# Kernel optimization log

Measured on AMD Instinct MI355X. Metric: run time of the kernel, lower is better.

The kernel has to match this reference:

```python
import jax, jax.numpy as jnp
import numpy as np

K_LAYERS = 10
ALPHA = 0.1
N_NODES = 100000
N_EDGES = 500000
N_PATHS = 3
D = 128
HID = 128


def setup_inputs() -> dict:
    key = jax.random.key(0)
    k1, k2, k3, k4 = jax.random.split(key, 4)
    h = jax.random.normal(k1, (N_NODES, D), dtype=jnp.float32)
    edges = jax.random.randint(k2, (N_PATHS, 2, N_EDGES), 0, N_NODES, dtype=jnp.int64)
    W1 = jax.random.normal(k3, (D, HID), dtype=jnp.float32) * (1.0 / np.sqrt(D))
    b1 = jnp.zeros((HID,), dtype=jnp.float32)
    w2 = jax.random.normal(k4, (HID, 1), dtype=jnp.float32) * (1.0 / np.sqrt(HID))
    return {"h": h, "edges": edges, "W1": W1, "b1": b1, "w2": w2}


def _appnp(h0, src, dst):
    # DGL APPNPConv (eval mode, no dropout): symmetric degree normalization,
    # K steps of h <- (1-alpha) * D_in^{-1/2} A D_out^{-1/2} h + alpha * h0
    n = h0.shape[0]
    ones = jnp.ones(src.shape[0], dtype=h0.dtype)
    out_deg = jnp.clip(jax.ops.segment_sum(ones, src, num_segments=n), 1.0)
    in_deg = jnp.clip(jax.ops.segment_sum(ones, dst, num_segments=n), 1.0)
    norm_s = out_deg ** -0.5  # [N]
    norm_d = in_deg ** -0.5   # [N]

    def step(x, _):
        msg = (x * norm_s[:, None])[src]                       # [E, D] gather
        agg = jax.ops.segment_sum(msg, dst, num_segments=n)    # [N, D] scatter-add
        x = (1.0 - ALPHA) * (agg * norm_d[:, None]) + ALPHA * h0
        return x, None

    x, _ = jax.lax.scan(step, h0, None, length=K_LAYERS)
    return x


def reference(h, edges, W1, b1, w2):
    src = edges[:, 0, :]  # [P, E]
    dst = edges[:, 1, :]
    # one APPNP propagation per meta-path, vmapped over the P axis
    z = jax.vmap(lambda s, d: _appnp(h, s, d))(src, dst)  # [P, N, D]
    z = jnp.transpose(z, (1, 0, 2))                        # [N, P, D]
    # semantic attention: small MLP -> mean over nodes -> softmax over paths
    w = jnp.tanh(z @ W1 + b1) @ w2   # [N, P, 1]
    w = w.mean(axis=0)               # [P, 1]
    beta = jax.nn.softmax(w, axis=0) # [P, 1]
    return (beta[None, :, :] * z).sum(axis=1)  # [N, D]
```

## Files before the change

kernel.cpp:

```cpp
#include <hip/hip_runtime.h>
#include <math.h>

#define N_NODES 100000
#define N_EDGES 500000
#define N_PATHS 3
#define DIM 128
#define K_LAYERS 10
#define NBLK_PER_PATH ((N_NODES + 255) / 256)

typedef __attribute__((ext_vector_type(8))) short bf16x8;
typedef __attribute__((ext_vector_type(4))) float f32x4;

__global__ __launch_bounds__(256) void deg_kernel(const int* __restrict__ edges,
                                                  int* __restrict__ degS,
                                                  int* __restrict__ degD) {
    int idx = blockIdx.x * 256 + threadIdx.x;
    if (idx < N_PATHS * N_EDGES) {
        int p = idx / N_EDGES;
        int e = idx - p * N_EDGES;
        const int* src = edges + (size_t)p * 2 * N_EDGES;
        const int* dst = src + N_EDGES;
        atomicAdd(&degS[p * N_NODES + src[e]], 1);
        atomicAdd(&degD[p * N_NODES + dst[e]], 1);
    }
}

__global__ __launch_bounds__(256) void norm_kernel(const int* __restrict__ degS,
                                                   const int* __restrict__ degD,
                                                   float* __restrict__ norm_s,
                                                   float* __restrict__ norm_d) {
    int n = blockIdx.x * 256 + threadIdx.x;
    if (n < N_PATHS * N_NODES) {
        norm_s[n] = 1.0f / sqrtf(fmaxf((float)degS[n], 1.0f));
        norm_d[n] = 1.0f / sqrtf(fmaxf((float)degD[n], 1.0f));
    }
}

__global__ __launch_bounds__(256) void blocksum_kernel(const int* __restrict__ cnt,
                                                       int* __restrict__ bsum) {
    int b = blockIdx.x;
    int p = b / NBLK_PER_PATH;
    int lb = b - p * NBLK_PER_PATH;
    int idx = lb * 256 + threadIdx.x;
    int v = (idx < N_NODES) ? cnt[p * N_NODES + idx] : 0;
#pragma unroll
    for (int off = 32; off; off >>= 1) v += __shfl_xor(v, off);
    __shared__ int ws[4];
    if ((threadIdx.x & 63) == 0) ws[threadIdx.x >> 6] = v;
    __syncthreads();
    if (threadIdx.x == 0) bsum[b] = ws[0] + ws[1] + ws[2] + ws[3];
}

__global__ __launch_bounds__(512) void bscan_kernel(int* __restrict__ bsum) {
    __shared__ int s[512];
    int p = blockIdx.x;
    int t = threadIdx.x;
    int v = (t < NBLK_PER_PATH) ? bsum[p * NBLK_PER_PATH + t] : 0;
    s[t] = v;
    __syncthreads();
    for (int off = 1; off < 512; off <<= 1) {
        int x = s[t];
        int a = (t >= off) ? s[t - off] : 0;
        __syncthreads();
        s[t] = x + a;
        __syncthreads();
    }
    if (t < NBLK_PER_PATH) bsum[p * NBLK_PER_PATH + t] = s[t] - v;
}

__global__ __launch_bounds__(256) void scan_write_kernel(const int* __restrict__ cnt,
                                                         const int* __restrict__ bsum,
                                                         int* __restrict__ row_ptr_all,
                                                         int* __restrict__ cursor_all) {
    __shared__ int s[256];
    int b = blockIdx.x;
    int p = b / NBLK_PER_PATH;
    int lb = b - p * NBLK_PER_PATH;
    int idx = lb * 256 + threadIdx.x;
    int t = threadIdx.x;
    int v = (idx < N_NODES) ? cnt[p * N_NODES + idx] : 0;
    s[t] = v;
    __syncthreads();
    for (int off = 1; off < 256; off <<= 1) {
        int x = s[t];
        int a = (t >= off) ? s[t - off] : 0;
        __syncthreads();
        s[t] = x + a;
        __syncthreads();
    }
    int excl = s[t] - v + bsum[b];
    if (idx < N_NODES) {
        row_ptr_all[p * (N_NODES + 1) + idx] = excl;
        cursor_all[p * N_NODES + idx] = excl;
        if (idx == N_NODES - 1)
            row_ptr_all[p * (N_NODES + 1) + N_NODES] = excl + v;
    }
}

__global__ __launch_bounds__(256) void fill_kernel(const int* __restrict__ edges,
                                                   const float* __restrict__ norm_s,
                                                   const float* __restrict__ norm_d,
                                                   int* __restrict__ cursor,
                                                   int2* __restrict__ cw) {
    int idx = blockIdx.x * 256 + threadIdx.x;
    if (idx < N_PATHS * N_EDGES) {
        int p = idx / N_EDGES;
        int e = idx - p * N_EDGES;
        const int* src = edges + (size_t)p * 2 * N_EDGES;
        const int* dst = src + N_EDGES;
        int s = src[e], d = dst[e];
        int pos = atomicAdd(&cursor[p * N_NODES + d], 1);
        float w = 0.9f * norm_s[p * N_NODES + s] * norm_d[p * N_NODES + d];
        cw[(size_t)p * N_EDGES + pos] = make_int2(s, __float_as_int(w));
    }
}

__device__ __forceinline__ unsigned bf16pack(float a, float b) {
    unsigned ua = __float_as_uint(a), ub = __float_as_uint(b);
    ua = (ua + 0x7fffu + ((ua >> 16) & 1)) >> 16;
    ub = (ub + 0x7fffu + ((ub >> 16) & 1)) >> 16;
    return ua | (ub << 16);
}

__global__ __launch_bounds__(256) void cast_kernel(const float4* __restrict__ in,
                                                   ushort4* __restrict__ outp) {
    int idx = blockIdx.x * 256 + threadIdx.x;
    if (idx < N_NODES * DIM / 4) {
        float4 v = in[idx];
        ushort4 o;
        unsigned u;
        u = __float_as_uint(v.x); o.x = (unsigned short)((u + 0x7fff + ((u >> 16) & 1)) >> 16);
        u = __float_as_uint(v.y); o.y = (unsigned short)((u + 0x7fff + ((u >> 16) & 1)) >> 16);
        u = __float_as_uint(v.z); o.z = (unsigned short)((u + 0x7fff + ((u >> 16) & 1)) >> 16);
        u = __float_as_uint(v.w); o.w = (unsigned short)((u + 0x7fff + ((u >> 16) & 1)) >> 16);
        outp[idx] = o;
    }
}

__global__ __launch_bounds__(256) void w1t_kernel(const float* __restrict__ W1,
                                                  unsigned short* __restrict__ W1t) {
    int idx = blockIdx.x * 256 + threadIdx.x;
    if (idx < DIM * DIM) {
        int c = idx >> 7, k = idx & 127;
        unsigned u = __float_as_uint(W1[k * DIM + c]);
        W1t[idx] = (unsigned short)((u + 0x7fff + ((u >> 16) & 1)) >> 16);
    }
}

template <int OUT_F32>
__global__ __launch_bounds__(256) void prop_kernel(const unsigned short* __restrict__ xin,
                                                   size_t in_stride,
                                                   const float* __restrict__ h0f,
                                                   void* __restrict__ xout,
                                                   const int* __restrict__ row_ptr,
                                                   const int2* __restrict__ cw) {
    int wid  = threadIdx.x >> 6;
    int lane = threadIdx.x & 63;
    int q    = lane >> 4;
    int ql   = lane & 15;
    int nodeBase = blockIdx.x * 16 + wid * 4;
    int p  = nodeBase / N_NODES;
    int nb = nodeBase - p * N_NODES;
    const int*  rp   = row_ptr + p * (N_NODES + 1);
    const int2* cwp  = cw + (size_t)p * N_EDGES;
    const uint4* xin4 = (const uint4*)(xin + (size_t)p * in_stride);

    int rv = 0;
    if (lane < 5) rv = rp[nb + lane];
    int beg = __shfl(rv, q);
    int end = __shfl(rv, q + 1);
    int deg = end - beg;
    int myNode = nb + q;
    int maxd = deg;
    maxd = max(maxd, __shfl_xor(maxd, 16));
    maxd = max(maxd, __shfl_xor(maxd, 32));

    float a0 = 0.f, a1 = 0.f, a2 = 0.f, a3 = 0.f;
    float a4 = 0.f, a5 = 0.f, a6 = 0.f, a7 = 0.f;

    for (int base = 0; base < maxd; base += 16) {
        int2 e = make_int2(0, 0);
        if (base + ql < deg) e = cwp[beg + base + ql];
        int lim = maxd - base; if (lim > 16) lim = 16;
#pragma unroll 4
        for (int j = 0; j < lim; ++j) {
            int lsrc = (lane & 48) | j;
            int   c = __shfl(e.x, lsrc);
            float w = __int_as_float(__shfl(e.y, lsrc));
            if (base + j < deg) {
                uint4 v = xin4[(size_t)c * 16 + ql];
                a0 = fmaf(w, __uint_as_float(v.x << 16), a0);
                a1 = fmaf(w, __uint_as_float(v.x & 0xffff0000u), a1);
                a2 = fmaf(w, __uint_as_float(v.y << 16), a2);
                a3 = fmaf(w, __uint_as_float(v.y & 0xffff0000u), a3);
                a4 = fmaf(w, __uint_as_float(v.z << 16), a4);
                a5 = fmaf(w, __uint_as_float(v.z & 0xffff0000u), a5);
                a6 = fmaf(w, __uint_as_float(v.w << 16), a6);
                a7 = fmaf(w, __uint_as_float(v.w & 0xffff0000u), a7);
            }
        }
    }

    const float4* h4 = (const float4*)(h0f + (size_t)myNode * DIM);
    float4 h0v = h4[ql * 2];
    float4 h1v = h4[ql * 2 + 1];
    a0 += 0.1f * h0v.x; a1 += 0.1f * h0v.y; a2 += 0.1f * h0v.z; a3 += 0.1f * h0v.w;
    a4 += 0.1f * h1v.x; a5 += 0.1f * h1v.y; a6 += 0.1f * h1v.z; a7 += 0.1f * h1v.w;

    size_t row = (size_t)p * N_NODES + myNode;
    if (OUT_F32) {
        float4* zo = (float4*)xout + row * 32;
        zo[ql * 2]     = make_float4(a0, a1, a2, a3);
        zo[ql * 2 + 1] = make_float4(a4, a5, a6, a7);
    } else {
        uint4 o;
        o.x = bf16pack(a0, a1);
        o.y = bf16pack(a2, a3);
        o.z = bf16pack(a4, a5);
        o.w = bf16pack(a6, a7);
        ((uint4*)xout)[row * 16 + ql] = o;
    }
}

__device__ __forceinline__ float fast_tanh(float x) {
    float e = __expf(2.0f * x);
    return 1.0f - 2.0f / (e + 1.0f);
}

__global__ __launch_bounds__(256) void attn_kernel(const float* __restrict__ z,
                                                   const unsigned short* __restrict__ W1t,
                                                   const float* __restrict__ b1,
                                                   const float* __restrict__ w2,
                                                   float* __restrict__ wsum) {
    const int wid  = threadIdx.x >> 6;
    const int lane = threadIdx.x & 63;
    const int c0   = lane & 15;
    const int kh   = lane >> 4;

    const bf16x8* w1t8 = (const bf16x8*)W1t;
    bf16x8 Bf[8][4];
#pragma unroll
    for (int nt = 0; nt < 8; ++nt)
#pragma unroll
        for (int ks = 0; ks < 4; ++ks)
            Bf[nt][ks] = w1t8[(nt * 16 + c0) * 16 + ks * 4 + kh];

    float b1v[8], w2v[8];
#pragma unroll
    for (int nt = 0; nt < 8; ++nt) {
        b1v[nt] = b1[nt * 16 + c0];
        w2v[nt] = w2[nt * 16 + c0];
    }

    float accP0 = 0.f, accP1 = 0.f, accP2 = 0.f;
    const int NTILES = N_PATHS * N_NODES / 16;
    const int TPP    = N_NODES / 16;
    const int stride = gridDim.x * 4;
    const float4* zf4 = (const float4*)z;

    for (int t = blockIdx.x * 4 + wid; t < NTILES; t += stride) {
        size_t rbase = ((size_t)t * 16 + c0) * 32 + kh * 2;
        bf16x8 Af[4];
#pragma unroll
        for (int ks = 0; ks < 4; ++ks) {
            float4 x0 = zf4[rbase + ks * 8];
            float4 x1 = zf4[rbase + ks * 8 + 1];
            union { uint4 u; bf16x8 v; } cv;
            cv.u.x = bf16pack(x0.x, x0.y);
            cv.u.y = bf16pack(x0.z, x0.w);
            cv.u.z = bf16pack(x1.x, x1.y);
            cv.u.w = bf16pack(x1.z, x1.w);
            Af[ks] = cv.v;
        }
        f32x4 acc[8];
#pragma unroll
        for (int nt = 0; nt < 8; ++nt) acc[nt] = (f32x4){0.f, 0.f, 0.f, 0.f};
#pragma unroll
        for (int nt = 0; nt < 8; ++nt)
#pragma unroll
            for (int ks = 0; ks < 4; ++ks)
                acc[nt] = __builtin_amdgcn_mfma_f32_16x16x32_bf16(Af[ks], Bf[nt][ks], acc[nt], 0, 0, 0);

        float psum = 0.f;
#pragma unroll
        for (int nt = 0; nt < 8; ++nt) {
            psum += fast_tanh(acc[nt][0] + b1v[nt]) * w2v[nt];
            psum += fast_tanh(acc[nt][1] + b1v[nt]) * w2v[nt];
            psum += fast_tanh(acc[nt][2] + b1v[nt]) * w2v[nt];
            psum += fast_tanh(acc[nt][3] + b1v[nt]) * w2v[nt];
        }
#pragma unroll
        for (int off = 32; off; off >>= 1) psum += __shfl_xor(psum, off);
        if (lane == 0) {
            int p = t / TPP;
            if (p == 0) accP0 += psum;
            else if (p == 1) accP1 += psum;
            else accP2 += psum;
        }
    }
    if (lane == 0) {
        if (accP0 != 0.f) atomicAdd(&wsum[0], accP0);
        if (accP1 != 0.f) atomicAdd(&wsum[1], accP1);
        if (accP2 != 0.f) atomicAdd(&wsum[2], accP2);
    }
}

__global__ void beta_kernel(const float* __restrict__ wsum, float* __restrict__ beta) {
    if (threadIdx.x == 0 && blockIdx.x == 0) {
        float w0 = wsum[0] * (1.0f / N_NODES);
        float w1 = wsum[1] * (1.0f / N_NODES);
        float w2v = wsum[2] * (1.0f / N_NODES);
        float m = fmaxf(w0, fmaxf(w1, w2v));
        float e0 = expf(w0 - m), e1 = expf(w1 - m), e2 = expf(w2v - m);
        float inv = 1.0f / (e0 + e1 + e2);
        beta[0] = e0 * inv;
        beta[1] = e1 * inv;
        beta[2] = e2 * inv;
    }
}

__global__ __launch_bounds__(256) void combine_kernel(const float4* __restrict__ z4,
                                                      const float* __restrict__ beta,
                                                      float4* __restrict__ out4) {
    size_t idx = (size_t)blockIdx.x * 256 + threadIdx.x;
    const size_t M = (size_t)N_NODES * 32;
    if (idx < M) {
        float b0 = beta[0], b1 = beta[1], b2 = beta[2];
        float4 a = z4[idx];
        float4 b = z4[M + idx];
        float4 c = z4[2 * M + idx];
        float4 o;
        o.x = b0 * a.x + b1 * b.x + b2 * c.x;
        o.y = b0 * a.y + b1 * b.y + b2 * c.y;
        o.z = b0 * a.z + b1 * b.z + b2 * c.z;
        o.w = b0 * a.w + b1 * b.w + b2 * c.w;
        out4[idx] = o;
    }
}

extern "C" void kernel_launch(void* const* d_in, const int* in_sizes, int n_in,
                              void* d_out, int out_size, void* d_ws, size_t ws_size,
                              hipStream_t stream) {
    const float* h     = (const float*)d_in[0];
    const int*   edges = (const int*)d_in[1];
    const float* W1    = (const float*)d_in[2];
    const float* b1    = (const float*)d_in[3];
    const float* w2    = (const float*)d_in[4];
    float* out = (float*)d_out;

    char* ws = (char*)d_ws;
    float* z = (float*)ws;               ws += (size_t)N_PATHS * N_NODES * DIM * 4;
    unsigned short* buf0 = (unsigned short*)ws; ws += (size_t)N_PATHS * N_NODES * DIM * 2;
    int2* cw = (int2*)ws;                ws += (size_t)N_PATHS * N_EDGES * 8;
    int* row_ptr = (int*)ws;             ws += (size_t)N_PATHS * (N_NODES + 1) * 4 + 12;
    int* cursor = (int*)ws;              ws += (size_t)N_PATHS * N_NODES * 4;
    float* norm_s = (float*)ws;          ws += (size_t)N_PATHS * N_NODES * 4;
    float* norm_d = (float*)ws;          ws += (size_t)N_PATHS * N_NODES * 4;
    int* degS = (int*)ws;                ws += (size_t)N_PATHS * N_NODES * 4;
    int* degD = (int*)ws;                ws += (size_t)N_PATHS * N_NODES * 4;
    int* bsum = (int*)ws;                ws += (size_t)N_PATHS * NBLK_PER_PATH * 4;
    float* wsum = (float*)ws;            ws += 4 * 4;
    float* beta = (float*)ws;            ws += 4 * 4;
    unsigned short* W1t = (unsigned short*)ws; ws += (size_t)DIM * DIM * 2;
    unsigned short* buf1 = (unsigned short*)z;
    unsigned short* hb   = (unsigned short*)z + (size_t)N_PATHS * N_NODES * DIM;

    const size_t PSTRIDE = (size_t)N_NODES * DIM;

    hipMemsetAsync(degS, 0, (size_t)2 * N_PATHS * N_NODES * 4, stream);
    deg_kernel<<<(N_PATHS * N_EDGES + 255) / 256, 256, 0, stream>>>(edges, degS, degD);
    norm_kernel<<<(N_PATHS * N_NODES + 255) / 256, 256, 0, stream>>>(degS, degD, norm_s, norm_d);
    blocksum_kernel<<<N_PATHS * NBLK_PER_PATH, 256, 0, stream>>>(degD, bsum);
    bscan_kernel<<<N_PATHS, 512, 0, stream>>>(bsum);
    scan_write_kernel<<<N_PATHS * NBLK_PER_PATH, 256, 0, stream>>>(degD, bsum, row_ptr, cursor);
    fill_kernel<<<(N_PATHS * N_EDGES + 255) / 256, 256, 0, stream>>>(edges, norm_s, norm_d, cursor, cw);

    cast_kernel<<<(N_NODES * DIM / 4 + 255) / 256, 256, 0, stream>>>(
        (const float4*)h, (ushort4*)hb);
    w1t_kernel<<<(DIM * DIM + 255) / 256, 256, 0, stream>>>(W1, W1t);

    const int pgrid = N_PATHS * N_NODES / 16;
    prop_kernel<0><<<pgrid, 256, 0, stream>>>(hb, 0, h, buf0, row_ptr, cw);
    for (int i = 1; i <= 8; ++i) {
        const unsigned short* src_b = (i & 1) ? buf0 : buf1;
        unsigned short* dst_b       = (i & 1) ? buf1 : buf0;
        prop_kernel<0><<<pgrid, 256, 0, stream>>>(src_b, PSTRIDE, h, dst_b, row_ptr, cw);
    }
    prop_kernel<1><<<pgrid, 256, 0, stream>>>(buf0, PSTRIDE, h, z, row_ptr, cw);

    hipMemsetAsync(wsum, 0, 3 * 4, stream);
    attn_kernel<<<512, 256, 0, stream>>>(z, W1t, b1, w2, wsum);
    beta_kernel<<<1, 64, 0, stream>>>(wsum, beta);
    combine_kernel<<<(N_NODES * 32 + 255) / 256, 256, 0, stream>>>(
        (const float4*)z, beta, (float4*)out);
}
```

Before: 1.196 ms.

## Shard degree counters and CSR fill cursors across eight replicas

Degree counting and CSR fill now spread their atomics over eight shard-private counter arrays, chosen by block index, instead of one shared array. A reduce kernel sums the shards to get norms and total in-degree. A new cursor-init kernel gives each shard its own sub-range inside each destination row. This is meant to cut atomic contention and serialization on hot nodes. In exchange it adds memset traffic, two extra passes over the 8x counter arrays, and reuses buf0 as scratch space for them.

```diff
diff --git a/kernel.cpp b/kernel.cpp
--- a/kernel.cpp
+++ b/kernel.cpp
@@ -7,32 +7,43 @@
 #define DIM 128
 #define K_LAYERS 10
 #define NBLK_PER_PATH ((N_NODES + 255) / 256)
+#define PN (N_PATHS * N_NODES)
+#define NSHARD 8
 
 typedef __attribute__((ext_vector_type(8))) short bf16x8;
 typedef __attribute__((ext_vector_type(4))) float f32x4;
 
 __global__ __launch_bounds__(256) void deg_kernel(const int* __restrict__ edges,
-                                                  int* __restrict__ degS,
-                                                  int* __restrict__ degD) {
+                                                  int* __restrict__ degS8,
+                                                  int* __restrict__ degD8) {
     int idx = blockIdx.x * 256 + threadIdx.x;
+    int shard = blockIdx.x & (NSHARD - 1);
     if (idx < N_PATHS * N_EDGES) {
         int p = idx / N_EDGES;
         int e = idx - p * N_EDGES;
         const int* src = edges + (size_t)p * 2 * N_EDGES;
         const int* dst = src + N_EDGES;
-        atomicAdd(&degS[p * N_NODES + src[e]], 1);
-        atomicAdd(&degD[p * N_NODES + dst[e]], 1);
-    }
-}
-
-__global__ __launch_bounds__(256) void norm_kernel(const int* __restrict__ degS,
-                                                   const int* __restrict__ degD,
-                                                   float* __restrict__ norm_s,
-                                                   float* __restrict__ norm_d) {
-    int n = blockIdx.x * 256 + threadIdx.x;
-    if (n < N_PATHS * N_NODES) {
-        norm_s[n] = 1.0f / sqrtf(fmaxf((float)degS[n], 1.0f));
-        norm_d[n] = 1.0f / sqrtf(fmaxf((float)degD[n], 1.0f));
+        atomicAdd(&degS8[shard * PN + p * N_NODES + src[e]], 1);
+        atomicAdd(&degD8[shard * PN + p * N_NODES + dst[e]], 1);
+    }
+}
+
+__global__ __launch_bounds__(256) void norm_reduce_kernel(const int* __restrict__ degS8,
+                                                          const int* __restrict__ degD8,
+                                                          float* __restrict__ norm_s,
+                                                          float* __restrict__ norm_d,
+                                                          int* __restrict__ degD_tot) {
+    int i = blockIdx.x * 256 + threadIdx.x;
+    if (i < PN) {
+        int sS = 0, sD = 0;
+#pragma unroll
+        for (int s = 0; s < NSHARD; ++s) {
+            sS += degS8[s * PN + i];
+            sD += degD8[s * PN + i];
+        }
+        norm_s[i] = 1.0f / sqrtf(fmaxf((float)sS, 1.0f));
+        norm_d[i] = 1.0f / sqrtf(fmaxf((float)sD, 1.0f));
+        degD_tot[i] = sD;
     }
 }
 
@@ -70,8 +81,7 @@
 
 __global__ __launch_bounds__(256) void scan_write_kernel(const int* __restrict__ cnt,
                                                          const int* __restrict__ bsum,
-                                                         int* __restrict__ row_ptr_all,
-                                                         int* __restrict__ cursor_all) {
+                                                         int* __restrict__ row_ptr_all) {
     __shared__ int s[256];
     int b = blockIdx.x;
     int p = b / NBLK_PER_PATH;
@@ -91,25 +101,41 @@
     int excl = s[t] - v + bsum[b];
     if (idx < N_NODES) {
         row_ptr_all[p * (N_NODES + 1) + idx] = excl;
-        cursor_all[p * N_NODES + idx] = excl;
         if (idx == N_NODES - 1)
             row_ptr_all[p * (N_NODES + 1) + N_NODES] = excl + v;
+    }
+}
+
+__global__ __launch_bounds__(256) void cursor_init_kernel(const int* __restrict__ row_ptr_all,
+                                                          const int* __restrict__ degD8,
+                                                          int* __restrict__ cursor8) {
+    int i = blockIdx.x * 256 + threadIdx.x;
+    if (i < PN) {
+        int p = i / N_NODES;
+        int n = i - p * N_NODES;
+        int c = row_ptr_all[p * (N_NODES + 1) + n];
+#pragma unroll
+        for (int s = 0; s < NSHARD; ++s) {
+            cursor8[s * PN + i] = c;
+            c += degD8[s * PN + i];
+        }
     }
 }
 
 __global__ __launch_bounds__(256) void fill_kernel(const int* __restrict__ edges,
                                                    const float* __restrict__ norm_s,
                                                    const float* __restrict__ norm_d,
-                                                   int* __restrict__ cursor,
+                                                   int* __restrict__ cursor8,
                                                    int2* __restrict__ cw) {
     int idx = blockIdx.x * 256 + threadIdx.x;
+    int shard = blockIdx.x & (NSHARD - 1);
     if (idx < N_PATHS * N_EDGES) {
         int p = idx / N_EDGES;
         int e = idx - p * N_EDGES;
         const int* src = edges + (size_t)p * 2 * N_EDGES;
         const int* dst = src + N_EDGES;
         int s = src[e], d = dst[e];
-        int pos = atomicAdd(&cursor[p * N_NODES + d], 1);
+        int pos = atomicAdd(&cursor8[shard * PN + p * N_NODES + d], 1);
         float w = 0.9f * norm_s[p * N_NODES + s] * norm_d[p * N_NODES + d];
         cw[(size_t)p * N_EDGES + pos] = make_int2(s, __float_as_int(w));
     }
@@ -353,27 +379,29 @@
     unsigned short* buf0 = (unsigned short*)ws; ws += (size_t)N_PATHS * N_NODES * DIM * 2;
     int2* cw = (int2*)ws;                ws += (size_t)N_PATHS * N_EDGES * 8;
     int* row_ptr = (int*)ws;             ws += (size_t)N_PATHS * (N_NODES + 1) * 4 + 12;
-    int* cursor = (int*)ws;              ws += (size_t)N_PATHS * N_NODES * 4;
-    float* norm_s = (float*)ws;          ws += (size_t)N_PATHS * N_NODES * 4;
-    float* norm_d = (float*)ws;          ws += (size_t)N_PATHS * N_NODES * 4;
-    int* degS = (int*)ws;                ws += (size_t)N_PATHS * N_NODES * 4;
-    int* degD = (int*)ws;                ws += (size_t)N_PATHS * N_NODES * 4;
+    float* norm_s = (float*)ws;          ws += (size_t)PN * 4;
+    float* norm_d = (float*)ws;          ws += (size_t)PN * 4;
     int* bsum = (int*)ws;                ws += (size_t)N_PATHS * NBLK_PER_PATH * 4;
     float* wsum = (float*)ws;            ws += 4 * 4;
     float* beta = (float*)ws;            ws += 4 * 4;
     unsigned short* W1t = (unsigned short*)ws; ws += (size_t)DIM * DIM * 2;
+    int* degS8    = (int*)buf0;
+    int* degD8    = degS8 + (size_t)NSHARD * PN;
+    int* cursor8  = degD8 + (size_t)NSHARD * PN;
+    int* degD_tot = cursor8 + (size_t)NSHARD * PN;
     unsigned short* buf1 = (unsigned short*)z;
     unsigned short* hb   = (unsigned short*)z + (size_t)N_PATHS * N_NODES * DIM;
 
     const size_t PSTRIDE = (size_t)N_NODES * DIM;
 
-    hipMemsetAsync(degS, 0, (size_t)2 * N_PATHS * N_NODES * 4, stream);
-    deg_kernel<<<(N_PATHS * N_EDGES + 255) / 256, 256, 0, stream>>>(edges, degS, degD);
-    norm_kernel<<<(N_PATHS * N_NODES + 255) / 256, 256, 0, stream>>>(degS, degD, norm_s, norm_d);
-    blocksum_kernel<<<N_PATHS * NBLK_PER_PATH, 256, 0, stream>>>(degD, bsum);
+    hipMemsetAsync(degS8, 0, (size_t)2 * NSHARD * PN * 4, stream);
+    deg_kernel<<<(N_PATHS * N_EDGES + 255) / 256, 256, 0, stream>>>(edges, degS8, degD8);
+    norm_reduce_kernel<<<(PN + 255) / 256, 256, 0, stream>>>(degS8, degD8, norm_s, norm_d, degD_tot);
+    blocksum_kernel<<<N_PATHS * NBLK_PER_PATH, 256, 0, stream>>>(degD_tot, bsum);
     bscan_kernel<<<N_PATHS, 512, 0, stream>>>(bsum);
-    scan_write_kernel<<<N_PATHS * NBLK_PER_PATH, 256, 0, stream>>>(degD, bsum, row_ptr, cursor);
-    fill_kernel<<<(N_PATHS * N_EDGES + 255) / 256, 256, 0, stream>>>(edges, norm_s, norm_d, cursor, cw);
+    scan_write_kernel<<<N_PATHS * NBLK_PER_PATH, 256, 0, stream>>>(degD_tot, bsum, row_ptr);
+    cursor_init_kernel<<<(PN + 255) / 256, 256, 0, stream>>>(row_ptr, degD8, cursor8);
+    fill_kernel<<<(N_PATHS * N_EDGES + 255) / 256, 256, 0, stream>>>(edges, norm_s, norm_d, cursor8, cw);
 
     cast_kernel<<<(N_NODES * DIM / 4 + 255) / 256, 256, 0, stream>>>(
         (const float4*)h, (ushort4*)hb);
```

After: 1.192 ms. About the same (-0.3%).

## Replace global-atomic degree count with LDS histograms and read bf16 anchor

Applied to the files above, without the earlier changes.

Degree counting no longer uses global atomics. It now builds shared-memory histograms per node range and edge chunk, then a reduce kernel sums the partials and computes both normalisations at once. This removes a memset and the separate norm kernel, and reuses the buf0 region as scratch. The intermediate propagation steps now read the alpha*h0 term from the bf16 copy of h instead of fp32, which halves that traffic but adds rounding error to the anchor term. The final step still uses fp32 h.

```diff
diff --git a/kernel.cpp b/kernel.cpp
--- a/kernel.cpp
+++ b/kernel.cpp
@@ -7,33 +7,59 @@
 #define DIM 128
 #define K_LAYERS 10
 #define NBLK_PER_PATH ((N_NODES + 255) / 256)
+#define PN (N_PATHS * N_NODES)
+#define HRANGE 16384
+#define NRANGE ((N_NODES + HRANGE - 1) / HRANGE)
+#define BPG 8
 
 typedef __attribute__((ext_vector_type(8))) short bf16x8;
 typedef __attribute__((ext_vector_type(4))) float f32x4;
 
-__global__ __launch_bounds__(256) void deg_kernel(const int* __restrict__ edges,
-                                                  int* __restrict__ degS,
-                                                  int* __restrict__ degD) {
-    int idx = blockIdx.x * 256 + threadIdx.x;
-    if (idx < N_PATHS * N_EDGES) {
-        int p = idx / N_EDGES;
-        int e = idx - p * N_EDGES;
-        const int* src = edges + (size_t)p * 2 * N_EDGES;
-        const int* dst = src + N_EDGES;
-        atomicAdd(&degS[p * N_NODES + src[e]], 1);
-        atomicAdd(&degD[p * N_NODES + dst[e]], 1);
-    }
-}
-
-__global__ __launch_bounds__(256) void norm_kernel(const int* __restrict__ degS,
-                                                   const int* __restrict__ degD,
-                                                   float* __restrict__ norm_s,
-                                                   float* __restrict__ norm_d) {
-    int n = blockIdx.x * 256 + threadIdx.x;
-    if (n < N_PATHS * N_NODES) {
-        norm_s[n] = 1.0f / sqrtf(fmaxf((float)degS[n], 1.0f));
-        norm_d[n] = 1.0f / sqrtf(fmaxf((float)degD[n], 1.0f));
-    }
+__device__ __forceinline__ float bflo(unsigned u) { return __uint_as_float(u << 16); }
+__device__ __forceinline__ float bfhi(unsigned u) { return __uint_as_float(u & 0xffff0000u); }
+
+__global__ __launch_bounds__(256) void hist_kernel(const int* __restrict__ edges,
+                                                   int* __restrict__ partial) {
+    __shared__ int hist[HRANGE];
+    int g = blockIdx.x / BPG;
+    int b = blockIdx.x - g * BPG;
+    int r = g % NRANGE;
+    int pt = g / NRANGE;
+    int p = pt >> 1, t = pt & 1;
+    for (int i = threadIdx.x; i < HRANGE; i += 256) hist[i] = 0;
+    __syncthreads();
+    const int* arr = edges + ((size_t)p * 2 + t) * N_EDGES;
+    int lo = r * HRANGE;
+    const int chunk = N_EDGES / BPG;
+    int beg = b * chunk;
+    for (int i = beg + threadIdx.x; i < beg + chunk; i += 256) {
+        int v = arr[i] - lo;
+        if ((unsigned)v < HRANGE) atomicAdd(&hist[v], 1);
+    }
+    __syncthreads();
+    int* outp = partial + ((size_t)g * BPG + b) * HRANGE;
+    for (int i = threadIdx.x; i < HRANGE; i += 256) outp[i] = hist[i];
+}
+
+__global__ __launch_bounds__(256) void deg_reduce_kernel(const int* __restrict__ partial,
+                                                         float* __restrict__ norm_s,
+                                                         float* __restrict__ norm_d,
+                                                         int* __restrict__ degD_tot) {
+    int i = blockIdx.x * 256 + threadIdx.x;
+    if (i >= PN) return;
+    int p = i / N_NODES, n = i - p * N_NODES;
+    int r = n / HRANGE, off = n - r * HRANGE;
+    const int* ps = partial + (((size_t)(p * 2 + 0) * NRANGE + r) * BPG) * HRANGE + off;
+    const int* pd = partial + (((size_t)(p * 2 + 1) * NRANGE + r) * BPG) * HRANGE + off;
+    int sS = 0, sD = 0;
+#pragma unroll
+    for (int b = 0; b < BPG; ++b) {
+        sS += ps[(size_t)b * HRANGE];
+        sD += pd[(size_t)b * HRANGE];
+    }
+    norm_s[i] = 1.0f / sqrtf(fmaxf((float)sS, 1.0f));
+    norm_d[i] = 1.0f / sqrtf(fmaxf((float)sD, 1.0f));
+    degD_tot[i] = sD;
 }
 
 __global__ __launch_bounds__(256) void blocksum_kernel(const int* __restrict__ cnt,
@@ -147,10 +173,10 @@
     }
 }
 
-template <int OUT_F32>
+template <int OUT_F32, int H_BF16>
 __global__ __launch_bounds__(256) void prop_kernel(const unsigned short* __restrict__ xin,
                                                    size_t in_stride,
-                                                   const float* __restrict__ h0f,
+                                                   const void* __restrict__ anchor,
                                                    void* __restrict__ xout,
                                                    const int* __restrict__ row_ptr,
                                                    const int2* __restrict__ cw) {
@@ -189,23 +215,31 @@
             float w = __int_as_float(__shfl(e.y, lsrc));
             if (base + j < deg) {
                 uint4 v = xin4[(size_t)c * 16 + ql];
-                a0 = fmaf(w, __uint_as_float(v.x << 16), a0);
-                a1 = fmaf(w, __uint_as_float(v.x & 0xffff0000u), a1);
-                a2 = fmaf(w, __uint_as_float(v.y << 16), a2);
-                a3 = fmaf(w, __uint_as_float(v.y & 0xffff0000u), a3);
-                a4 = fmaf(w, __uint_as_float(v.z << 16), a4);
-                a5 = fmaf(w, __uint_as_float(v.z & 0xffff0000u), a5);
-                a6 = fmaf(w, __uint_as_float(v.w << 16), a6);
-                a7 = fmaf(w, __uint_as_float(v.w & 0xffff0000u), a7);
+                a0 = fmaf(w, bflo(v.x), a0);
+                a1 = fmaf(w, bfhi(v.x), a1);
+                a2 = fmaf(w, bflo(v.y), a2);
+                a3 = fmaf(w, bfhi(v.y), a3);
+                a4 = fmaf(w, bflo(v.z), a4);
+                a5 = fmaf(w, bfhi(v.z), a5);
+                a6 = fmaf(w, bflo(v.w), a6);
+                a7 = fmaf(w, bfhi(v.w), a7);
             }
         }
     }
 
-    const float4* h4 = (const float4*)(h0f + (size_t)myNode * DIM);
-    float4 h0v = h4[ql * 2];
-    float4 h1v = h4[ql * 2 + 1];
-    a0 += 0.1f * h0v.x; a1 += 0.1f * h0v.y; a2 += 0.1f * h0v.z; a3 += 0.1f * h0v.w;
-    a4 += 0.1f * h1v.x; a5 += 0.1f * h1v.y; a6 += 0.1f * h1v.z; a7 += 0.1f * h1v.w;
+    if (H_BF16) {
+        uint4 hv = ((const uint4*)anchor)[(size_t)myNode * 16 + ql];
+        a0 += 0.1f * bflo(hv.x); a1 += 0.1f * bfhi(hv.x);
+        a2 += 0.1f * bflo(hv.y); a3 += 0.1f * bfhi(hv.y);
+        a4 += 0.1f * bflo(hv.z); a5 += 0.1f * bfhi(hv.z);
+        a6 += 0.1f * bflo(hv.w); a7 += 0.1f * bfhi(hv.w);
+    } else {
+        const float4* h4 = (const float4*)anchor + (size_t)myNode * 32;
+        float4 h0v = h4[ql * 2];
+        float4 h1v = h4[ql * 2 + 1];
+        a0 += 0.1f * h0v.x; a1 += 0.1f * h0v.y; a2 += 0.1f * h0v.z; a3 += 0.1f * h0v.w;
+        a4 += 0.1f * h1v.x; a5 += 0.1f * h1v.y; a6 += 0.1f * h1v.z; a7 += 0.1f * h1v.w;
+    }
 
     size_t row = (size_t)p * N_NODES + myNode;
     if (OUT_F32) {
@@ -353,26 +387,25 @@
     unsigned short* buf0 = (unsigned short*)ws; ws += (size_t)N_PATHS * N_NODES * DIM * 2;
     int2* cw = (int2*)ws;                ws += (size_t)N_PATHS * N_EDGES * 8;
     int* row_ptr = (int*)ws;             ws += (size_t)N_PATHS * (N_NODES + 1) * 4 + 12;
-    int* cursor = (int*)ws;              ws += (size_t)N_PATHS * N_NODES * 4;
-    float* norm_s = (float*)ws;          ws += (size_t)N_PATHS * N_NODES * 4;
-    float* norm_d = (float*)ws;          ws += (size_t)N_PATHS * N_NODES * 4;
-    int* degS = (int*)ws;                ws += (size_t)N_PATHS * N_NODES * 4;
-    int* degD = (int*)ws;                ws += (size_t)N_PATHS * N_NODES * 4;
+    float* norm_s = (float*)ws;          ws += (size_t)PN * 4;
+    float* norm_d = (float*)ws;          ws += (size_t)PN * 4;
     int* bsum = (int*)ws;                ws += (size_t)N_PATHS * NBLK_PER_PATH * 4;
     float* wsum = (float*)ws;            ws += 4 * 4;
     float* beta = (float*)ws;            ws += 4 * 4;
     unsigned short* W1t = (unsigned short*)ws; ws += (size_t)DIM * DIM * 2;
+    int* partial  = (int*)buf0;
+    int* degD_tot = partial + (size_t)3 * 2 * NRANGE * BPG * HRANGE;
+    int* cursor   = degD_tot + PN;
     unsigned short* buf1 = (unsigned short*)z;
     unsigned short* hb   = (unsigned short*)z + (size_t)N_PATHS * N_NODES * DIM;
 
     const size_t PSTRIDE = (size_t)N_NODES * DIM;
 
-    hipMemsetAsync(degS, 0, (size_t)2 * N_PATHS * N_NODES * 4, stream);
-    deg_kernel<<<(N_PATHS * N_EDGES + 255) / 256, 256, 0, stream>>>(edges, degS, degD);
-    norm_kernel<<<(N_PATHS * N_NODES + 255) / 256, 256, 0, stream>>>(degS, degD, norm_s, norm_d);
-    blocksum_kernel<<<N_PATHS * NBLK_PER_PATH, 256, 0, stream>>>(degD, bsum);
+    hist_kernel<<<3 * 2 * NRANGE * BPG, 256, 0, stream>>>(edges, partial);
+    deg_reduce_kernel<<<(PN + 255) / 256, 256, 0, stream>>>(partial, norm_s, norm_d, degD_tot);
+    blocksum_kernel<<<N_PATHS * NBLK_PER_PATH, 256, 0, stream>>>(degD_tot, bsum);
     bscan_kernel<<<N_PATHS, 512, 0, stream>>>(bsum);
-    scan_write_kernel<<<N_PATHS * NBLK_PER_PATH, 256, 0, stream>>>(degD, bsum, row_ptr, cursor);
+    scan_write_kernel<<<N_PATHS * NBLK_PER_PATH, 256, 0, stream>>>(degD_tot, bsum, row_ptr, cursor);
     fill_kernel<<<(N_PATHS * N_EDGES + 255) / 256, 256, 0, stream>>>(edges, norm_s, norm_d, cursor, cw);
 
     cast_kernel<<<(N_NODES * DIM / 4 + 255) / 256, 256, 0, stream>>>(
@@ -380,13 +413,13 @@
     w1t_kernel<<<(DIM * DIM + 255) / 256, 256, 0, stream>>>(W1, W1t);
 
     const int pgrid = N_PATHS * N_NODES / 16;
-    prop_kernel<0><<<pgrid, 256, 0, stream>>>(hb, 0, h, buf0, row_ptr, cw);
+    prop_kernel<0, 1><<<pgrid, 256, 0, stream>>>(hb, 0, hb, buf0, row_ptr, cw);
     for (int i = 1; i <= 8; ++i) {
         const unsigned short* src_b = (i & 1) ? buf0 : buf1;
         unsigned short* dst_b       = (i & 1) ? buf1 : buf0;
-        prop_kernel<0><<<pgrid, 256, 0, stream>>>(src_b, PSTRIDE, h, dst_b, row_ptr, cw);
-    }
-    prop_kernel<1><<<pgrid, 256, 0, stream>>>(buf0, PSTRIDE, h, z, row_ptr, cw);
+        prop_kernel<0, 1><<<pgrid, 256, 0, stream>>>(src_b, PSTRIDE, hb, dst_b, row_ptr, cw);
+    }
+    prop_kernel<1, 0><<<pgrid, 256, 0, stream>>>(buf0, PSTRIDE, h, z, row_ptr, cw);
 
     hipMemsetAsync(wsum, 0, 3 * 4, stream);
     attn_kernel<<<512, 256, 0, stream>>>(z, W1t, b1, w2, wsum);
```

New measurement: 1.110 ms. -7.2%, faster.
